# Performance work log

Hardware: AMD Instinct MI355X
Metric: run time of the kernel (lower is better)

The kernel has to match this reference:

```python
import jax, jax.numpy as jnp
import numpy as np

D, DH, NH = 256, 32, 8  # d_model, d_head, n_heads


def conv2d(x, w, stride=1, padding='VALID', groups=1):
    return jax.lax.conv_general_dilated(
        x, w, (stride, stride), padding,
        feature_group_count=groups,
        dimension_numbers=('NCHW', 'OIHW', 'NCHW'))


def bn2d(x, p):
    # p: [4, C] rows = gamma, beta, running_mean, running_var (inference-mode BN)
    g, b, m, v = p[0], p[1], p[2], p[3]
    inv = g / jnp.sqrt(v + 1e-5)
    return (x - m[:, None, None]) * inv[:, None, None] + b[:, None, None]


def gelu(x):
    return jax.nn.gelu(x, approximate=False)  # torch nn.GELU default (erf)


def to_heads(x):
    # [b, heads*d, h, w] -> [b, h*w, heads, d]
    b, c, h, w = x.shape
    return x.reshape(b, NH, DH, h * w).transpose(0, 3, 1, 2)


def from_heads(x, h, w):
    # [b, h*w, heads, d] -> [b, heads*d, h, w]
    b = x.shape[0]
    return x.transpose(0, 2, 3, 1).reshape(b, NH * DH, h, w)


def linear_attention(q, k, v, eps=1e-6):
    # LoFTR linear attention: phi(x) = elu(x) + 1
    Q = jax.nn.elu(q) + 1.0
    K = jax.nn.elu(k) + 1.0
    L = v.shape[1]
    vn = v / L
    KV = jnp.einsum('nshd,nshv->nhdv', K, vn)
    Z = 1.0 / (jnp.einsum('nlhd,nhd->nlh', Q, K.sum(axis=1)) + eps)
    return jnp.einsum('nlhd,nhdv,nlh->nlhv', Q, KV, Z) * L


def upsample_bilinear_ac(x, s):
    # bilinear, align_corners=True, integer scale factor s (separable H then W)
    def interp(a, axis):
        n_in = a.shape[axis]
        n_out = n_in * s
        pos = jnp.arange(n_out) * ((n_in - 1) / (n_out - 1))
        i0 = jnp.floor(pos).astype(jnp.int32)
        i1 = jnp.minimum(i0 + 1, n_in - 1)
        t = (pos - i0.astype(pos.dtype)).astype(a.dtype)
        sh = [1] * a.ndim
        sh[axis] = n_out
        t = t.reshape(sh)
        return jnp.take(a, i0, axis=axis) * (1 - t) + jnp.take(a, i1, axis=axis) * t
    return interp(interp(x, 2), 3)


def _bn_params(key, c):
    k1, k2, k3, k4 = jax.random.split(key, 4)
    return jnp.stack([
        1.0 + 0.05 * jax.random.normal(k1, (c,)),
        0.05 * jax.random.normal(k2, (c,)),
        0.05 * jax.random.normal(k3, (c,)),
        0.5 + jax.random.uniform(k4, (c,))]).astype(jnp.float32)


def setup_inputs() -> dict:
    key = jax.random.key(0)
    ks = jax.random.split(key, 24)
    B, H, W = 4, 128, 128
    Dm = 4 * D  # MB hidden dim (mlp_ratio=4)

    def w(k, shape, fan_in):
        return (jax.random.normal(k, shape) / np.sqrt(fan_in)).astype(jnp.float32)

    return {
        'x0': jax.random.normal(ks[0], (B, D, H, W), dtype=jnp.float32),
        'scale_weight': jnp.ones((3,), jnp.float32),
        'bn_pre': _bn_params(ks[1], D),
        'wq1': w(ks[2], (D, D, 1, 1), D),
        'wk1': w(ks[3], (D, D, 1, 1), D),
        'wv1': w(ks[4], (D, D, 1, 1), D),
        'wq2': w(ks[5], (D, D, 2, 2), D * 4),
        'wk2': w(ks[6], (D, D, 2, 2), D * 4),
        'wv2': w(ks[7], (D, D, 2, 2), D * 4),
        'wq3': w(ks[8], (D, D, 4, 4), D * 16),
        'wk3': w(ks[9], (D, D, 4, 4), D * 16),
        'wv3': w(ks[10], (D, D, 4, 4), D * 16),
        'merge_w': w(ks[11], (D, D, 1, 1), D),
        'merge_b': 0.01 * jax.random.normal(ks[12], (D,), dtype=jnp.float32),
        'mb_w1': w(ks[13], (Dm, D, 1, 1), D),
        'bn_mb1': _bn_params(ks[14], Dm),
        'mb_wdw': w(ks[15], (Dm, 1, 3, 3), 9),
        'bn_mb2': _bn_params(ks[16], Dm),
        'mb_w2': w(ks[17], (D, Dm, 1, 1), Dm),
        'bn_mb3': _bn_params(ks[18], D),
    }


def reference(x0, scale_weight, bn_pre, wq1, wk1, wv1, wq2, wk2, wv2,
              wq3, wk3, wv3, merge_w, merge_b, mb_w1, bn_mb1, mb_wdw,
              bn_mb2, mb_w2, bn_mb3):
    b, d, h, w = x0.shape
    xn = gelu(bn2d(x0, bn_pre))  # x1 is None -> x1 = x0, shared pre_normact
    # multi-scale conv QKV projections (strides 1, 2, 4)
    q1 = to_heads(conv2d(xn, wq1)); k1 = to_heads(conv2d(xn, wk1)); v1 = to_heads(conv2d(xn, wv1))
    q2 = to_heads(conv2d(xn, wq2, 2)); k2 = to_heads(conv2d(xn, wk2, 2)); v2 = to_heads(conv2d(xn, wv2, 2))
    q3 = to_heads(conv2d(xn, wq3, 4)); k3 = to_heads(conv2d(xn, wk3, 4)); v3 = to_heads(conv2d(xn, wv3, 4))
    o1 = from_heads(linear_attention(q1, k1, v1), h, w)
    o2 = from_heads(linear_attention(q2, k2, v2), h // 2, w // 2)
    o3 = from_heads(linear_attention(q3, k3, v3), h // 4, w // 4)
    o2 = upsample_bilinear_ac(o2, 2)
    o3 = upsample_bilinear_ac(o3, 4)
    sw = jax.nn.softmax(scale_weight)
    message = sw[0] * o1 + sw[1] * o2 + sw[2] * o3
    x = x0 + conv2d(message, merge_w) + merge_b[:, None, None]  # DropPath(0) = id
    # MB mlp: 1x1 expand -> BN -> GELU -> 3x3 depthwise -> BN -> GELU -> 1x1 -> BN
    hm = gelu(bn2d(conv2d(x, mb_w1), bn_mb1))
    hm = gelu(bn2d(conv2d(hm, mb_wdw, 1, ((1, 1), (1, 1)), groups=mb_wdw.shape[0]), bn_mb2))
    mlp_out = bn2d(conv2d(hm, mb_w2), bn_mb3)
    return x + mlp_out
```

## Files before the change

### kernel.cpp

```cpp
#include <hip/hip_runtime.h>
#include <hip/hip_bf16.h>

typedef __attribute__((ext_vector_type(4))) float f32x4;
typedef __attribute__((ext_vector_type(8))) short short8;
typedef unsigned int u32;
typedef unsigned short u16;

__device__ __forceinline__ float bf2f(u16 x) { return __uint_as_float(((u32)x) << 16); }
__device__ __forceinline__ u16 f2bf(float f) {
  u32 u = __float_as_uint(f);
  return (u16)((u + 0x7fffu + ((u >> 16) & 1u)) >> 16);
}
__device__ __forceinline__ float gelu_f(float x) { return 0.5f * x * (1.f + erff(x * 0.7071067811865475f)); }
__device__ __forceinline__ float phi_f(float x) { return x > 0.f ? x + 1.f : __expf(x); }
__device__ __forceinline__ void load8f(const __hip_bfloat16* p, float* f) {
  ushort4 a = *(const ushort4*)p, b = *(const ushort4*)(p + 4);
  f[0] = bf2f(a.x); f[1] = bf2f(a.y); f[2] = bf2f(a.z); f[3] = bf2f(a.w);
  f[4] = bf2f(b.x); f[5] = bf2f(b.y); f[6] = bf2f(b.z); f[7] = bf2f(b.w);
}
__device__ __forceinline__ void gload16(const void* g, void* l) {
  __builtin_amdgcn_global_load_lds((const __attribute__((address_space(1))) u32*)g,
                                   (__attribute__((address_space(3))) u32*)l, 16, 0, 0);
}

static constexpr size_t MiB = 1048576ull;
static constexpr size_t OFF_BNP_S = 0, OFF_BNP_T = 1024;
static constexpr size_t OFF_BN1_S = 2048, OFF_BN1_T = 6144;
static constexpr size_t OFF_BN2_S = 10240, OFF_BN2_T = 14336;
static constexpr size_t OFF_BN3_S = 18432, OFF_BN3_T = 19456;
static constexpr size_t OFF_WDW   = 20480;
static constexpr size_t OFF_KV    = 57344;
static constexpr size_t OFF_KSUM  = 450560;
static constexpr size_t OFF_W     = 524288;
static constexpr size_t WF1 = 0;
static constexpr size_t WF2 = 196608;
static constexpr size_t WF3 = 983040;
static constexpr size_t WE_MRG = 4128768;
static constexpr size_t WE_MB1 = 4194304;
static constexpr size_t WE_MB2 = 4456448;
static constexpr size_t OFF_XN    = 20 * MiB;
static constexpr size_t OFF_O1    = 52 * MiB;
static constexpr size_t OFF_O2    = 84 * MiB;
static constexpr size_t OFF_O3    = 92 * MiB;
static constexpr size_t OFF_QKV2  = 96 * MiB;
static constexpr size_t OFF_QKV3  = 120 * MiB;
static constexpr size_t OFF_PART  = 126 * MiB;
static constexpr size_t OFF_QKV1C = 126 * MiB;
static constexpr size_t OFF_MSG   = 128 * MiB;
static constexpr size_t OFF_XB    = 20 * MiB;
static constexpr size_t OFF_HM1   = 52 * MiB;
static constexpr size_t OFF_HM2   = 116 * MiB;
static constexpr size_t WS_NEED   = 180 * MiB;

__global__ __launch_bounds__(256) void fillf(float* p, int n, float v) {
  for (int i = blockIdx.x * 256 + threadIdx.x; i < n; i += gridDim.x * 256) p[i] = v;
}

__global__ __launch_bounds__(256) void bnprep(const float* __restrict__ bn,
                                              float* __restrict__ s, float* __restrict__ t, int C) {
  int c = blockIdx.x * 256 + threadIdx.x;
  if (c >= C) return;
  float g = bn[c], b = bn[C + c], m = bn[2 * C + c], v = bn[3 * C + c];
  float sc = g * rsqrtf(v + 1e-5f);
  s[c] = sc; t[c] = b - m * sc;
}

__global__ __launch_bounds__(256) void wdwprep(const float* __restrict__ w, float* __restrict__ out) {
  int g = blockIdx.x * 256 + threadIdx.x;
  if (g >= 9216) return;
  int c = g & 1023, p = g >> 10;
  out[p * 1024 + c] = w[c * 9 + p];
}

__global__ __launch_bounds__(256)
void wprep_all(const float* q1, const float* k1, const float* v1,
               const float* q2, const float* k2, const float* v2,
               const float* q3, const float* k3, const float* v3,
               const float* mrg, const float* m1, const float* m2,
               __hip_bfloat16* __restrict__ pool) {
  int g = blockIdx.x * 256 + threadIdx.x;
  if (g >= 4718592) return;
  const float* src; int C, S; int loc; size_t base;
  if (g < 196608)      { int seg = g / 65536;   src = seg == 0 ? q1 : seg == 1 ? k1 : v1; C = 256; S = 1; base = 0;       loc = g - seg * 65536; }
  else if (g < 983040) { int r = g - 196608; int seg = r / 262144; src = seg == 0 ? q2 : seg == 1 ? k2 : v2; C = 256; S = 2; base = 196608;  loc = r - seg * 262144; }
  else if (g < 4128768){ int r = g - 983040; int seg = r / 1048576; src = seg == 0 ? q3 : seg == 1 ? k3 : v3; C = 256; S = 4; base = 983040; loc = r - seg * 1048576; }
  else if (g < 4194304){ src = mrg; C = 256; S = 1; base = 4128768; loc = g - 4128768; }
  else if (g < 4456448){ src = m1; C = 256; S = 1; base = 4194304; loc = g - 4194304; }
  else                 { src = m2; C = 1024; S = 1; base = 4456448; loc = g - 4456448; }
  (void)base;
  int K = C * S * S;
  int o = loc / K, kk = loc - o * K;
  int c = kk % C, p = kk / C;
  pool[g] = __float2bfloat16(src[((size_t)o * C + c) * S * S + p]);
}

__global__ __launch_bounds__(256) void pre_normact(const float* __restrict__ x0, const float* __restrict__ s,
                                                   const float* __restrict__ t, __hip_bfloat16* __restrict__ xn) {
  __shared__ u16 lds[64 * 256];
  const int tid = threadIdx.x;
  const int p0 = blockIdx.x * 64;
  const int b = p0 >> 14, pin = p0 & 16383;
  const float sc = s[tid], sh = t[tid];
  const float* src = x0 + (((size_t)(b * 256 + tid)) << 14) + pin;
  #pragma unroll 4
  for (int j = 0; j < 64; j += 4) {
    float4 v = *(const float4*)(src + j);
    lds[(j + 0) * 256 + tid] = f2bf(gelu_f(v.x * sc + sh));
    lds[(j + 1) * 256 + tid] = f2bf(gelu_f(v.y * sc + sh));
    lds[(j + 2) * 256 + tid] = f2bf(gelu_f(v.z * sc + sh));
    lds[(j + 3) * 256 + tid] = f2bf(gelu_f(v.w * sc + sh));
  }
  __syncthreads();
  const uint4* lsrc = (const uint4*)lds;
  uint4* dst = (uint4*)((u16*)xn + (size_t)p0 * 256);
  #pragma unroll
  for (int i = 0; i < 8; ++i) dst[i * 256 + tid] = lsrc[i * 256 + tid];
}

template <int S, int EPI>
__global__ __launch_bounds__(256)
void gemm_bt(const __hip_bfloat16* __restrict__ A, const __hip_bfloat16* __restrict__ Bw,
             __hip_bfloat16* __restrict__ Cout, int N, int K, int ldb,
             const float* __restrict__ p0, const float* __restrict__ p1,
             const float* __restrict__ xsrc, float* __restrict__ xout, int ksplit) {
  __shared__ __hip_bfloat16 As[2][128 * 64];
  __shared__ __hip_bfloat16 Bs[2][128 * 64];
  const int tid = threadIdx.x;
  const int wave = tid >> 6, lane = tid & 63;
  const int ntn = N >> 7;
  int blk = blockIdx.x;
  { int nwg = gridDim.x; if ((nwg & 7) == 0) { int cpx = nwg >> 3; blk = (blk & 7) * cpx + (blk >> 3); } }
  int kbeg = 0, kend = K;
  float* xo = xout;
  if constexpr (EPI == 7) {
    int tiles = gridDim.x / ksplit;
    int split = blk / tiles; blk -= split * tiles;
    int knum = K / ksplit;
    kbeg = split * knum; kend = kbeg + knum;
    int M = (tiles / ntn) << 7;
    xo = xout + (size_t)split * M * N;
  }
  const int bm = blk / ntn, bnn = blk % ntn;
  const int wr = wave >> 1, wc = wave & 1;
  const int r_lo = lane & 15, r_hi = lane >> 4;
  f32x4 acc[4][4] = {};

  const __hip_bfloat16* aptr[4];
  #pragma unroll
  for (int i = 0; i < 4; ++i) {
    int ci = i * 256 + tid;
    int row = ci >> 3, c8 = ci & 7;
    int m = bm * 128 + row;
    size_t pixbase;
    if constexpr (S == 1) pixbase = (size_t)m * K;
    else if constexpr (S == 2) { int b = m >> 12, y = (m >> 6) & 63, x = m & 63; pixbase = ((size_t)(b * 16384 + y * 256 + x * 2)) * 256; }
    else { int b = m >> 10, y = (m >> 5) & 31, x = m & 31; pixbase = ((size_t)(b * 16384 + y * 512 + x * 4)) * 256; }
    aptr[i] = A + pixbase + c8 * 8;
  }
  const __hip_bfloat16* bptr[4];
  #pragma unroll
  for (int i = 0; i < 4; ++i) {
    int ci = i * 256 + tid;
    int row = ci >> 3, c8 = ci & 7;
    bptr[i] = Bw + (size_t)(bnn * 128 + row) * ldb + c8 * 8;
  }
  const int lofs = wave * 64 * 8;

  auto aoff_of = [&](int k0) -> size_t {
    if constexpr (S == 1) return (size_t)k0;
    else { int pq = k0 >> 8; int dy = pq / S, dx = pq % S; return (size_t)(((dy << 7) + dx) << 8) + (k0 & 255); }
  };

  {
    size_t ao = aoff_of(kbeg);
    #pragma unroll
    for (int i = 0; i < 4; ++i)
      gload16(aptr[i] + ao, (void*)(As[0] + i * 2048 + lofs));
    #pragma unroll
    for (int i = 0; i < 4; ++i)
      gload16(bptr[i] + kbeg, (void*)(Bs[0] + i * 2048 + lofs));
  }
  __syncthreads();

  int cur = 0;
  for (int k0 = kbeg; k0 < kend; k0 += 64) {
    if (k0 + 64 < kend) {
      size_t ao = aoff_of(k0 + 64);
      #pragma unroll
      for (int i = 0; i < 4; ++i)
        gload16(aptr[i] + ao, (void*)(As[cur ^ 1] + i * 2048 + lofs));
      #pragma unroll
      for (int i = 0; i < 4; ++i)
        gload16(bptr[i] + k0 + 64, (void*)(Bs[cur ^ 1] + i * 2048 + lofs));
    }
    const __hip_bfloat16* Ab = As[cur];
    const __hip_bfloat16* Bb = Bs[cur];
    #pragma unroll
    for (int kk = 0; kk < 2; ++kk) {
      short8 af[4], bfr[4];
      #pragma unroll
      for (int mi = 0; mi < 4; ++mi)
        af[mi] = *(const short8*)(Ab + (wr * 64 + mi * 16 + r_lo) * 64 + kk * 32 + r_hi * 8);
      #pragma unroll
      for (int ni = 0; ni < 4; ++ni)
        bfr[ni] = *(const short8*)(Bb + (wc * 64 + ni * 16 + r_lo) * 64 + kk * 32 + r_hi * 8);
      #pragma unroll
      for (int mi = 0; mi < 4; ++mi)
        #pragma unroll
        for (int ni = 0; ni < 4; ++ni)
          acc[mi][ni] = __builtin_amdgcn_mfma_f32_16x16x32_bf16(af[mi], bfr[ni], acc[mi][ni], 0, 0, 0);
    }
    __syncthreads();
    cur ^= 1;
  }

  const int m_base = bm * 128 + wr * 64;
  const int n_base = bnn * 128 + wc * 64;
  #pragma unroll
  for (int mi = 0; mi < 4; ++mi) {
    const int row0 = m_base + mi * 16 + r_hi * 4;
    #pragma unroll
    for (int ni = 0; ni < 4; ++ni) {
      const int col = n_base + ni * 16 + r_lo;
      f32x4 v = acc[mi][ni];
      if constexpr (EPI == 0) {
        #pragma unroll
        for (int j = 0; j < 4; ++j)
          *((u16*)Cout + (size_t)(row0 + j) * N + col) = f2bf(v[j]);
      } else if constexpr (EPI == 1) {
        const float sc = p0[col], sh = p1[col];
        #pragma unroll
        for (int j = 0; j < 4; ++j)
          *((u16*)Cout + (size_t)(row0 + j) * N + col) = f2bf(gelu_f(v[j] * sc + sh));
      } else if constexpr (EPI == 2) {
        const int b = row0 >> 14, pix = row0 & 16383;
        const size_t nchw = (((size_t)(b * 256 + col)) << 14) + pix;
        const float bias = p0[col];
        float4 xv = *(const float4*)(xsrc + nchw);
        float r0 = v[0] + bias + xv.x, r1 = v[1] + bias + xv.y;
        float r2 = v[2] + bias + xv.z, r3 = v[3] + bias + xv.w;
        *(float4*)(xo + nchw) = make_float4(r0, r1, r2, r3);
        *((u16*)Cout + (size_t)(row0 + 0) * 256 + col) = f2bf(r0);
        *((u16*)Cout + (size_t)(row0 + 1) * 256 + col) = f2bf(r1);
        *((u16*)Cout + (size_t)(row0 + 2) * 256 + col) = f2bf(r2);
        *((u16*)Cout + (size_t)(row0 + 3) * 256 + col) = f2bf(r3);
      } else if constexpr (EPI == 7) {
        #pragma unroll
        for (int j = 0; j < 4; ++j)
          xo[(size_t)(row0 + j) * N + col] = v[j];
      } else {
        const int b = row0 >> 14, pix = row0 & 16383;
        const size_t nchw = (((size_t)(b * 256 + col)) << 14) + pix;
        const float sc = p0[col], sh = p1[col];
        float4 pv = *(const float4*)(xo + nchw);
        *(float4*)(xo + nchw) = make_float4(v[0] * sc + sh + pv.x, v[1] * sc + sh + pv.y,
                                            v[2] * sc + sh + pv.z, v[3] * sc + sh + pv.w);
      }
    }
  }
}

__global__ __launch_bounds__(256) void reduce_part(const float* __restrict__ P,
                                                   __hip_bfloat16* __restrict__ out, int MN) {
  int i = (blockIdx.x * 256 + threadIdx.x) * 4;
  if (i >= MN) return;
  float4 a = *(const float4*)(P + i);
  float4 b = *(const float4*)(P + MN + i);
  ushort4 o;
  o.x = f2bf(a.x + b.x); o.y = f2bf(a.y + b.y); o.z = f2bf(a.z + b.z); o.w = f2bf(a.w + b.w);
  *(ushort4*)((u16*)out + i) = o;
}

__global__ __launch_bounds__(256)
void kv_reduce(const __hip_bfloat16* __restrict__ Km, const __hip_bfloat16* __restrict__ Vm,
               float* __restrict__ KV, float* __restrict__ Ksum, int L, int nchunks, int ld) {
  __shared__ float Ks[16][32];
  __shared__ float Vs[16][32];
  const int tid = threadIdx.x;
  const int blk = blockIdx.x;
  const int chunk = blk % nchunks;
  const int bh = blk / nchunks;
  const int h = bh & 7, b = bh >> 3;
  const int d = tid >> 3, v0 = (tid & 7) << 2;
  const int lr = tid >> 4, lq = tid & 15;
  const int cq = (lq & 7) << 2;
  const bool isK = lq < 8;
  const __hip_bfloat16* src = isK ? Km : Vm;
  const int CL = L / nchunks;
  const size_t base = (size_t)(b * L + chunk * CL) * ld + h * 32 + cq;
  float a0 = 0, a1 = 0, a2 = 0, a3 = 0, ks = 0;
  for (int it = 0; it < CL; it += 16) {
    ushort4 u = *(const ushort4*)(src + base + (size_t)(it + lr) * ld);
    float f0 = bf2f(u.x), f1 = bf2f(u.y), f2 = bf2f(u.z), f3 = bf2f(u.w);
    if (isK) {
      Ks[lr][cq + 0] = phi_f(f0); Ks[lr][cq + 1] = phi_f(f1);
      Ks[lr][cq + 2] = phi_f(f2); Ks[lr][cq + 3] = phi_f(f3);
    } else {
      Vs[lr][cq + 0] = f0; Vs[lr][cq + 1] = f1; Vs[lr][cq + 2] = f2; Vs[lr][cq + 3] = f3;
    }
    __syncthreads();
    #pragma unroll
    for (int s = 0; s < 16; ++s) {
      float kk = Ks[s][d];
      ks += kk;
      float4 vv = *(const float4*)&Vs[s][v0];
      a0 += kk * vv.x; a1 += kk * vv.y; a2 += kk * vv.z; a3 += kk * vv.w;
    }
    __syncthreads();
  }
  float* kvp = KV + (size_t)bh * 1024 + d * 32 + v0;
  atomicAdd(kvp + 0, a0); atomicAdd(kvp + 1, a1);
  atomicAdd(kvp + 2, a2); atomicAdd(kvp + 3, a3);
  if ((tid & 7) == 0) atomicAdd(Ksum + bh * 32 + d, ks);
}

__global__ __launch_bounds__(256)
void attn_out(const __hip_bfloat16* __restrict__ Qm, const float* __restrict__ KV,
              const float* __restrict__ Ksum, __hip_bfloat16* __restrict__ O, int npg, int ld) {
  __shared__ float QL[32][32];
  __shared__ float KVL[32][32];
  __shared__ float KsL[32];
  const int tid = threadIdx.x;
  const int blk = blockIdx.x;
  const int pg = blk % npg, bh = blk / npg;
  const int h = bh & 7;
  const int L = npg << 5;
  const int m0 = (bh >> 3) * L + (pg << 5);
  *(float4*)&KVL[tid >> 3][(tid & 7) * 4] = *(const float4*)(KV + (size_t)bh * 1024 + tid * 4);
  if (tid < 32) KsL[tid] = Ksum[bh * 32 + tid];
  {
    const int p = tid >> 3, d4 = (tid & 7) * 4;
    ushort4 qu = *(const ushort4*)(Qm + (size_t)(m0 + p) * ld + h * 32 + d4);
    *(float4*)&QL[p][d4] = make_float4(phi_f(bf2f(qu.x)), phi_f(bf2f(qu.y)),
                                       phi_f(bf2f(qu.z)), phi_f(bf2f(qu.w)));
  }
  __syncthreads();
  const int p = tid >> 3, v0 = (tid & 7) * 4;
  float a0 = 0, a1 = 0, a2 = 0, a3 = 0, z = 0;
  #pragma unroll 8
  for (int d = 0; d < 32; ++d) {
    float q = QL[p][d];
    z += q * KsL[d];
    float4 kv = *(const float4*)&KVL[d][v0];
    a0 += q * kv.x; a1 += q * kv.y; a2 += q * kv.z; a3 += q * kv.w;
  }
  float zi = 1.f / (z + 1e-6f);
  ushort4 o;
  o.x = f2bf(a0 * zi); o.y = f2bf(a1 * zi); o.z = f2bf(a2 * zi); o.w = f2bf(a3 * zi);
  *(ushort4*)(O + (size_t)(m0 + p) * 256 + h * 32 + v0) = o;
}

__global__ __launch_bounds__(256)
void message_compose(const __hip_bfloat16* __restrict__ o1, const __hip_bfloat16* __restrict__ o2,
                     const __hip_bfloat16* __restrict__ o3, const float* __restrict__ sw,
                     __hip_bfloat16* __restrict__ msg) {
  const int g = blockIdx.x * 256 + threadIdx.x;
  const int c0 = (g & 31) << 3;
  const int pix = g >> 5;
  const int x = pix & 127, y = (pix >> 7) & 127, b = pix >> 14;
  float w0 = sw[0], w1 = sw[1], w2 = sw[2];
  float mx = fmaxf(w0, fmaxf(w1, w2));
  float e0 = __expf(w0 - mx), e1 = __expf(w1 - mx), e2 = __expf(w2 - mx);
  float inv = 1.f / (e0 + e1 + e2);
  float s0 = e0 * inv, s1 = e1 * inv, s2 = e2 * inv;

  float acc[8], f[8];
  load8f(o1 + (size_t)pix * 256 + c0, f);
  #pragma unroll
  for (int j = 0; j < 8; ++j) acc[j] = s0 * f[j];
  {
    float py = y * (63.f / 127.f); int y0 = (int)py; float ty = py - y0; int y1 = min(y0 + 1, 63);
    float px = x * (63.f / 127.f); int x0 = (int)px; float tx = px - x0; int x1 = min(x0 + 1, 63);
    float wtl = (1 - ty) * (1 - tx), wtr = (1 - ty) * tx, wbl = ty * (1 - tx), wbr = ty * tx;
    const __hip_bfloat16* base = o2 + (size_t)b * 4096 * 256 + c0;
    float f00[8], f01[8], f10[8], f11[8];
    load8f(base + ((size_t)y0 * 64 + x0) * 256, f00);
    load8f(base + ((size_t)y0 * 64 + x1) * 256, f01);
    load8f(base + ((size_t)y1 * 64 + x0) * 256, f10);
    load8f(base + ((size_t)y1 * 64 + x1) * 256, f11);
    #pragma unroll
    for (int j = 0; j < 8; ++j)
      acc[j] += s1 * (wtl * f00[j] + wtr * f01[j] + wbl * f10[j] + wbr * f11[j]);
  }
  {
    float py = y * (31.f / 127.f); int y0 = (int)py; float ty = py - y0; int y1 = min(y0 + 1, 31);
    float px = x * (31.f / 127.f); int x0 = (int)px; float tx = px - x0; int x1 = min(x0 + 1, 31);
    float wtl = (1 - ty) * (1 - tx), wtr = (1 - ty) * tx, wbl = ty * (1 - tx), wbr = ty * tx;
    const __hip_bfloat16* base = o3 + (size_t)b * 1024 * 256 + c0;
    float f00[8], f01[8], f10[8], f11[8];
    load8f(base + ((size_t)y0 * 32 + x0) * 256, f00);
    load8f(base + ((size_t)y0 * 32 + x1) * 256, f01);
    load8f(base + ((size_t)y1 * 32 + x0) * 256, f10);
    load8f(base + ((size_t)y1 * 32 + x1) * 256, f11);
    #pragma unroll
    for (int j = 0; j < 8; ++j)
      acc[j] += s2 * (wtl * f00[j] + wtr * f01[j] + wbl * f10[j] + wbr * f11[j]);
  }
  ushort4 oa, ob;
  oa.x = f2bf(acc[0]); oa.y = f2bf(acc[1]); oa.z = f2bf(acc[2]); oa.w = f2bf(acc[3]);
  ob.x = f2bf(acc[4]); ob.y = f2bf(acc[5]); ob.z = f2bf(acc[6]); ob.w = f2bf(acc[7]);
  *(ushort4*)(msg + (size_t)pix * 256 + c0) = oa;
  *(ushort4*)(msg + (size_t)pix * 256 + c0 + 4) = ob;
}

__global__ __launch_bounds__(256)
void dwconv(const __hip_bfloat16* __restrict__ hm1, const float* __restrict__ wdw,
            const float* __restrict__ s, const float* __restrict__ t, __hip_bfloat16* __restrict__ hm2) {
  const int g = blockIdx.x * 256 + threadIdx.x;
  const int c0 = (g & 127) << 3;
  const int pix = g >> 7;
  const int x = pix & 127, y = (pix >> 7) & 127, b = pix >> 14;
  float acc[8] = {0, 0, 0, 0, 0, 0, 0, 0};
  #pragma unroll
  for (int ky = 0; ky < 3; ++ky) {
    int yy = y + ky - 1;
    if ((unsigned)yy >= 128u) continue;
    #pragma unroll
    for (int kx = 0; kx < 3; ++kx) {
      int xx = x + kx - 1;
      if ((unsigned)xx >= 128u) continue;
      const __hip_bfloat16* p = hm1 + ((((size_t)b * 128 + yy) * 128 + xx) << 10) + c0;
      ushort4 ua = *(const ushort4*)p, ub = *(const ushort4*)(p + 4);
      float4 wa = *(const float4*)&wdw[(ky * 3 + kx) * 1024 + c0];
      float4 wb = *(const float4*)&wdw[(ky * 3 + kx) * 1024 + c0 + 4];
      acc[0] += bf2f(ua.x) * wa.x; acc[1] += bf2f(ua.y) * wa.y;
      acc[2] += bf2f(ua.z) * wa.z; acc[3] += bf2f(ua.w) * wa.w;
      acc[4] += bf2f(ub.x) * wb.x; acc[5] += bf2f(ub.y) * wb.y;
      acc[6] += bf2f(ub.z) * wb.z; acc[7] += bf2f(ub.w) * wb.w;
    }
  }
  float4 sa = *(const float4*)&s[c0], sb = *(const float4*)&s[c0 + 4];
  float4 ta = *(const float4*)&t[c0], tb = *(const float4*)&t[c0 + 4];
  ushort4 oa, ob;
  oa.x = f2bf(gelu_f(acc[0] * sa.x + ta.x)); oa.y = f2bf(gelu_f(acc[1] * sa.y + ta.y));
  oa.z = f2bf(gelu_f(acc[2] * sa.z + ta.z)); oa.w = f2bf(gelu_f(acc[3] * sa.w + ta.w));
  ob.x = f2bf(gelu_f(acc[4] * sb.x + tb.x)); ob.y = f2bf(gelu_f(acc[5] * sb.y + tb.y));
  ob.z = f2bf(gelu_f(acc[6] * sb.z + tb.z)); ob.w = f2bf(gelu_f(acc[7] * sb.w + tb.w));
  *(ushort4*)(hm2 + ((size_t)pix << 10) + c0) = oa;
  *(ushort4*)(hm2 + ((size_t)pix << 10) + c0 + 4) = ob;
}

extern "C" void kernel_launch(void* const* d_in, const int* in_sizes, int n_in,
                              void* d_out, int out_size, void* d_ws, size_t ws_size,
                              hipStream_t stream) {
  const float* x0      = (const float*)d_in[0];
  const float* scale_w = (const float*)d_in[1];
  const float* bn_pre  = (const float*)d_in[2];
  const float* wq1 = (const float*)d_in[3];
  const float* wk1 = (const float*)d_in[4];
  const float* wv1 = (const float*)d_in[5];
  const float* wq2 = (const float*)d_in[6];
  const float* wk2 = (const float*)d_in[7];
  const float* wv2 = (const float*)d_in[8];
  const float* wq3 = (const float*)d_in[9];
  const float* wk3 = (const float*)d_in[10];
  const float* wv3 = (const float*)d_in[11];
  const float* merge_w = (const float*)d_in[12];
  const float* merge_b = (const float*)d_in[13];
  const float* mb_w1   = (const float*)d_in[14];
  const float* bn_mb1  = (const float*)d_in[15];
  const float* mb_wdw  = (const float*)d_in[16];
  const float* bn_mb2  = (const float*)d_in[17];
  const float* mb_w2   = (const float*)d_in[18];
  const float* bn_mb3  = (const float*)d_in[19];
  (void)in_sizes; (void)n_in;

  if (ws_size < WS_NEED) {
    fillf<<<4096, 256, 0, stream>>>((float*)d_out, out_size, (float)(ws_size >> 20));
    return;
  }

  char* ws = (char*)d_ws;
  auto F  = [&](size_t off) { return (float*)(ws + off); };
  auto BF = [&](size_t off) { return (__hip_bfloat16*)(ws + off); };
  __hip_bfloat16* Wp = BF(OFF_W);
  float* KV = F(OFF_KV);
  float* KS = F(OFF_KSUM);
  float* Xout = (float*)d_out;

  bnprep<<<1, 256, 0, stream>>>(bn_pre, F(OFF_BNP_S), F(OFF_BNP_T), 256);
  bnprep<<<4, 256, 0, stream>>>(bn_mb1, F(OFF_BN1_S), F(OFF_BN1_T), 1024);
  bnprep<<<4, 256, 0, stream>>>(bn_mb2, F(OFF_BN2_S), F(OFF_BN2_T), 1024);
  bnprep<<<1, 256, 0, stream>>>(bn_mb3, F(OFF_BN3_S), F(OFF_BN3_T), 256);
  wdwprep<<<36, 256, 0, stream>>>(mb_wdw, F(OFF_WDW));
  wprep_all<<<18432, 256, 0, stream>>>(wq1, wk1, wv1, wq2, wk2, wv2, wq3, wk3, wv3,
                                       merge_w, mb_w1, mb_w2, Wp);
  hipMemsetAsync(ws + OFF_KV, 0, 405504, stream);

  pre_normact<<<1024, 256, 0, stream>>>(x0, F(OFF_BNP_S), F(OFF_BNP_T), BF(OFF_XN));

  gemm_bt<2, 0><<<768, 256, 0, stream>>>(BF(OFF_XN), Wp + WF2, BF(OFF_QKV2), 768, 1024, 1024,
                                         nullptr, nullptr, nullptr, nullptr, 1);
  gemm_bt<4, 7><<<384, 256, 0, stream>>>(BF(OFF_XN), Wp + WF3, nullptr, 768, 4096, 4096,
                                         nullptr, nullptr, nullptr, F(OFF_PART), 2);
  reduce_part<<<3072, 256, 0, stream>>>(F(OFF_PART), BF(OFF_QKV3), 4096 * 768);

  kv_reduce<<<256, 256, 0, stream>>>(BF(OFF_QKV2) + 256, BF(OFF_QKV2) + 512, KV + 32768, KS + 1024, 4096, 8, 768);
  kv_reduce<<<256, 256, 0, stream>>>(BF(OFF_QKV3) + 256, BF(OFF_QKV3) + 512, KV + 65536, KS + 2048, 1024, 8, 768);
  attn_out<<<4096, 256, 0, stream>>>(BF(OFF_QKV2), KV + 32768, KS + 1024, BF(OFF_O2), 128, 768);
  attn_out<<<1024, 256, 0, stream>>>(BF(OFF_QKV3), KV + 65536, KS + 2048, BF(OFF_O3), 32, 768);

  for (int c = 0; c < 4; ++c) {
    const __hip_bfloat16* Ac = BF(OFF_XN) + (size_t)c * 16384 * 256;
    gemm_bt<1, 0><<<768, 256, 0, stream>>>(Ac, Wp + WF1, BF(OFF_QKV1C), 768, 256, 256,
                                           nullptr, nullptr, nullptr, nullptr, 1);
    kv_reduce<<<512, 256, 0, stream>>>(BF(OFF_QKV1C) + 256, BF(OFF_QKV1C) + 512,
                                       KV + c * 8192, KS + c * 256, 16384, 64, 768);
    attn_out<<<4096, 256, 0, stream>>>(BF(OFF_QKV1C), KV + c * 8192, KS + c * 256,
                                       BF(OFF_O1) + (size_t)c * 16384 * 256, 512, 768);
  }

  message_compose<<<8192, 256, 0, stream>>>(BF(OFF_O1), BF(OFF_O2), BF(OFF_O3), scale_w, BF(OFF_MSG));
  gemm_bt<1, 2><<<1024, 256, 0, stream>>>(BF(OFF_MSG), Wp + WE_MRG, BF(OFF_XB), 256, 256, 256,
                                          merge_b, nullptr, x0, Xout, 1);

  for (int half = 0; half < 2; ++half) {
    const __hip_bfloat16* XBh = BF(OFF_XB) + (size_t)half * 32768 * 256;
    float* Xoh = Xout + (size_t)half * 2 * 256 * 16384;
    gemm_bt<1, 1><<<2048, 256, 0, stream>>>(XBh, Wp + WE_MB1, BF(OFF_HM1), 1024, 256, 256,
                                            F(OFF_BN1_S), F(OFF_BN1_T), nullptr, nullptr, 1);
    dwconv<<<16384, 256, 0, stream>>>(BF(OFF_HM1), F(OFF_WDW), F(OFF_BN2_S), F(OFF_BN2_T), BF(OFF_HM2));
    gemm_bt<1, 8><<<512, 256, 0, stream>>>(BF(OFF_HM2), Wp + WE_MB2, nullptr, 256, 1024, 1024,
                                           F(OFF_BN3_S), F(OFF_BN3_T), nullptr, Xoh, 1);
  }
}
```

Baseline: 1.047 ms.

## Restructure attn_out per-pixel all-heads, row-streaming dwconv, fold BN scale, larger QKV1 chunks

attn_out now has each thread compute all 32 output channels for one pixel and head, with the KV matrices for all 8 heads staged in padded LDS. This removes the per-head-block Q staging and uses fewer, larger blocks. dwconv streams down 16-row column segments per thread, keeping the weights in registers and reusing each loaded row for three output rows, which cuts redundant global loads. The BN2 scale is folded into the depthwise weights at prep time, and the QKV1 path is processed in 2 chunks of 2 images instead of 4, with MSG aliased onto the freed workspace. Register pressure rises (q[32], acc[32], w[72]) and dwconv parallelism drops to 256K threads.

```diff
diff --git a/kernel.cpp b/kernel.cpp
--- a/kernel.cpp
+++ b/kernel.cpp
@@ -17,6 +17,12 @@
   ushort4 a = *(const ushort4*)p, b = *(const ushort4*)(p + 4);
   f[0] = bf2f(a.x); f[1] = bf2f(a.y); f[2] = bf2f(a.z); f[3] = bf2f(a.w);
   f[4] = bf2f(b.x); f[5] = bf2f(b.y); f[6] = bf2f(b.z); f[7] = bf2f(b.w);
+}
+__device__ __forceinline__ void cvt8(uint4 u, float* f) {
+  f[0] = bf2f((u16)(u.x & 0xffff)); f[1] = bf2f((u16)(u.x >> 16));
+  f[2] = bf2f((u16)(u.y & 0xffff)); f[3] = bf2f((u16)(u.y >> 16));
+  f[4] = bf2f((u16)(u.z & 0xffff)); f[5] = bf2f((u16)(u.z >> 16));
+  f[6] = bf2f((u16)(u.w & 0xffff)); f[7] = bf2f((u16)(u.w >> 16));
 }
 __device__ __forceinline__ void gload16(const void* g, void* l) {
   __builtin_amdgcn_global_load_lds((const __attribute__((address_space(1))) u32*)g,
@@ -45,8 +51,8 @@
 static constexpr size_t OFF_QKV2  = 96 * MiB;
 static constexpr size_t OFF_QKV3  = 120 * MiB;
 static constexpr size_t OFF_PART  = 126 * MiB;
-static constexpr size_t OFF_QKV1C = 126 * MiB;
-static constexpr size_t OFF_MSG   = 128 * MiB;
+static constexpr size_t OFF_QKV1P = 126 * MiB;
+static constexpr size_t OFF_MSG   = 126 * MiB;
 static constexpr size_t OFF_XB    = 20 * MiB;
 static constexpr size_t OFF_HM1   = 52 * MiB;
 static constexpr size_t OFF_HM2   = 116 * MiB;
@@ -65,11 +71,12 @@
   s[c] = sc; t[c] = b - m * sc;
 }
 
-__global__ __launch_bounds__(256) void wdwprep(const float* __restrict__ w, float* __restrict__ out) {
+__global__ __launch_bounds__(256) void wdwprep(const float* __restrict__ w, const float* __restrict__ s,
+                                               float* __restrict__ out) {
   int g = blockIdx.x * 256 + threadIdx.x;
   if (g >= 9216) return;
   int c = g & 1023, p = g >> 10;
-  out[p * 1024 + c] = w[c * 9 + p];
+  out[p * 1024 + c] = w[c * 9 + p] * s[c];
 }
 
 __global__ __launch_bounds__(256)
@@ -80,14 +87,13 @@
                __hip_bfloat16* __restrict__ pool) {
   int g = blockIdx.x * 256 + threadIdx.x;
   if (g >= 4718592) return;
-  const float* src; int C, S; int loc; size_t base;
-  if (g < 196608)      { int seg = g / 65536;   src = seg == 0 ? q1 : seg == 1 ? k1 : v1; C = 256; S = 1; base = 0;       loc = g - seg * 65536; }
-  else if (g < 983040) { int r = g - 196608; int seg = r / 262144; src = seg == 0 ? q2 : seg == 1 ? k2 : v2; C = 256; S = 2; base = 196608;  loc = r - seg * 262144; }
-  else if (g < 4128768){ int r = g - 983040; int seg = r / 1048576; src = seg == 0 ? q3 : seg == 1 ? k3 : v3; C = 256; S = 4; base = 983040; loc = r - seg * 1048576; }
-  else if (g < 4194304){ src = mrg; C = 256; S = 1; base = 4128768; loc = g - 4128768; }
-  else if (g < 4456448){ src = m1; C = 256; S = 1; base = 4194304; loc = g - 4194304; }
-  else                 { src = m2; C = 1024; S = 1; base = 4456448; loc = g - 4456448; }
-  (void)base;
+  const float* src; int C, S; int loc;
+  if (g < 196608)      { int seg = g / 65536;   src = seg == 0 ? q1 : seg == 1 ? k1 : v1; C = 256; S = 1; loc = g - seg * 65536; }
+  else if (g < 983040) { int r = g - 196608; int seg = r / 262144; src = seg == 0 ? q2 : seg == 1 ? k2 : v2; C = 256; S = 2; loc = r - seg * 262144; }
+  else if (g < 4128768){ int r = g - 983040; int seg = r / 1048576; src = seg == 0 ? q3 : seg == 1 ? k3 : v3; C = 256; S = 4; loc = r - seg * 1048576; }
+  else if (g < 4194304){ src = mrg; C = 256; S = 1; loc = g - 4128768; }
+  else if (g < 4456448){ src = m1; C = 256; S = 1; loc = g - 4194304; }
+  else                 { src = m2; C = 1024; S = 1; loc = g - 4456448; }
   int K = C * S * S;
   int o = loc / K, kk = loc - o * K;
   int c = kk % C, p = kk / C;
@@ -316,38 +322,59 @@
 
 __global__ __launch_bounds__(256)
 void attn_out(const __hip_bfloat16* __restrict__ Qm, const float* __restrict__ KV,
-              const float* __restrict__ Ksum, __hip_bfloat16* __restrict__ O, int npg, int ld) {
-  __shared__ float QL[32][32];
-  __shared__ float KVL[32][32];
-  __shared__ float KsL[32];
+              const float* __restrict__ Ksum, __hip_bfloat16* __restrict__ O, int lshift, int ld) {
+  __shared__ float KVL[8 * 1156];
+  __shared__ float KsL[8 * 33];
   const int tid = threadIdx.x;
-  const int blk = blockIdx.x;
-  const int pg = blk % npg, bh = blk / npg;
-  const int h = bh & 7;
-  const int L = npg << 5;
-  const int m0 = (bh >> 3) * L + (pg << 5);
-  *(float4*)&KVL[tid >> 3][(tid & 7) * 4] = *(const float4*)(KV + (size_t)bh * 1024 + tid * 4);
-  if (tid < 32) KsL[tid] = Ksum[bh * 32 + tid];
-  {
-    const int p = tid >> 3, d4 = (tid & 7) * 4;
-    ushort4 qu = *(const ushort4*)(Qm + (size_t)(m0 + p) * ld + h * 32 + d4);
-    *(float4*)&QL[p][d4] = make_float4(phi_f(bf2f(qu.x)), phi_f(bf2f(qu.y)),
-                                       phi_f(bf2f(qu.z)), phi_f(bf2f(qu.w)));
+  const int m0 = blockIdx.x << 5;
+  const int bh0 = (m0 >> lshift) << 3;
+  #pragma unroll
+  for (int i = 0; i < 8; ++i) {
+    int id = i * 256 + tid;
+    int h = id >> 8, rem = id & 255;
+    int d = rem >> 3, vi = rem & 7;
+    float4 v = *(const float4*)(KV + (((size_t)(bh0 + h)) << 10) + rem * 4);
+    *(float4*)&KVL[h * 1156 + d * 36 + vi * 4] = v;
+  }
+  { int h = tid >> 5, d = tid & 31; KsL[h * 33 + d] = Ksum[(bh0 + h) * 32 + d]; }
+  const int p = tid >> 3, h = tid & 7;
+  const u16* qp = (const u16*)Qm + (size_t)(m0 + p) * ld + h * 32;
+  float q[32];
+  #pragma unroll
+  for (int i = 0; i < 4; ++i) {
+    uint4 u = *(const uint4*)(qp + i * 8);
+    q[i * 8 + 0] = phi_f(bf2f((u16)(u.x & 0xffff))); q[i * 8 + 1] = phi_f(bf2f((u16)(u.x >> 16)));
+    q[i * 8 + 2] = phi_f(bf2f((u16)(u.y & 0xffff))); q[i * 8 + 3] = phi_f(bf2f((u16)(u.y >> 16)));
+    q[i * 8 + 4] = phi_f(bf2f((u16)(u.z & 0xffff))); q[i * 8 + 5] = phi_f(bf2f((u16)(u.z >> 16)));
+    q[i * 8 + 6] = phi_f(bf2f((u16)(u.w & 0xffff))); q[i * 8 + 7] = phi_f(bf2f((u16)(u.w >> 16)));
   }
   __syncthreads();
-  const int p = tid >> 3, v0 = (tid & 7) * 4;
-  float a0 = 0, a1 = 0, a2 = 0, a3 = 0, z = 0;
-  #pragma unroll 8
+  const float* kvh = &KVL[h * 1156];
+  const float* ksh = &KsL[h * 33];
+  float acc[32] = {};
+  float z = 0.f;
+  #pragma unroll
   for (int d = 0; d < 32; ++d) {
-    float q = QL[p][d];
-    z += q * KsL[d];
-    float4 kv = *(const float4*)&KVL[d][v0];
-    a0 += q * kv.x; a1 += q * kv.y; a2 += q * kv.z; a3 += q * kv.w;
+    float qd = q[d];
+    z += qd * ksh[d];
+    #pragma unroll
+    for (int vi = 0; vi < 8; ++vi) {
+      float4 kv = *(const float4*)&kvh[d * 36 + vi * 4];
+      acc[vi * 4 + 0] += qd * kv.x; acc[vi * 4 + 1] += qd * kv.y;
+      acc[vi * 4 + 2] += qd * kv.z; acc[vi * 4 + 3] += qd * kv.w;
+    }
   }
   float zi = 1.f / (z + 1e-6f);
-  ushort4 o;
-  o.x = f2bf(a0 * zi); o.y = f2bf(a1 * zi); o.z = f2bf(a2 * zi); o.w = f2bf(a3 * zi);
-  *(ushort4*)(O + (size_t)(m0 + p) * 256 + h * 32 + v0) = o;
+  u16* op = (u16*)O + (size_t)(m0 + p) * 256 + h * 32;
+  #pragma unroll
+  for (int i = 0; i < 4; ++i) {
+    uint4 o;
+    o.x = (u32)f2bf(acc[i * 8 + 0] * zi) | ((u32)f2bf(acc[i * 8 + 1] * zi) << 16);
+    o.y = (u32)f2bf(acc[i * 8 + 2] * zi) | ((u32)f2bf(acc[i * 8 + 3] * zi) << 16);
+    o.z = (u32)f2bf(acc[i * 8 + 4] * zi) | ((u32)f2bf(acc[i * 8 + 5] * zi) << 16);
+    o.w = (u32)f2bf(acc[i * 8 + 6] * zi) | ((u32)f2bf(acc[i * 8 + 7] * zi) << 16);
+    *(uint4*)(op + i * 8) = o;
+  }
 }
 
 __global__ __launch_bounds__(256)
@@ -405,39 +432,58 @@
 
 __global__ __launch_bounds__(256)
 void dwconv(const __hip_bfloat16* __restrict__ hm1, const float* __restrict__ wdw,
-            const float* __restrict__ s, const float* __restrict__ t, __hip_bfloat16* __restrict__ hm2) {
+            const float* __restrict__ t, __hip_bfloat16* __restrict__ hm2) {
   const int g = blockIdx.x * 256 + threadIdx.x;
   const int c0 = (g & 127) << 3;
-  const int pix = g >> 7;
-  const int x = pix & 127, y = (pix >> 7) & 127, b = pix >> 14;
-  float acc[8] = {0, 0, 0, 0, 0, 0, 0, 0};
-  #pragma unroll
-  for (int ky = 0; ky < 3; ++ky) {
-    int yy = y + ky - 1;
-    if ((unsigned)yy >= 128u) continue;
-    #pragma unroll
-    for (int kx = 0; kx < 3; ++kx) {
-      int xx = x + kx - 1;
-      if ((unsigned)xx >= 128u) continue;
-      const __hip_bfloat16* p = hm1 + ((((size_t)b * 128 + yy) * 128 + xx) << 10) + c0;
-      ushort4 ua = *(const ushort4*)p, ub = *(const ushort4*)(p + 4);
-      float4 wa = *(const float4*)&wdw[(ky * 3 + kx) * 1024 + c0];
-      float4 wb = *(const float4*)&wdw[(ky * 3 + kx) * 1024 + c0 + 4];
-      acc[0] += bf2f(ua.x) * wa.x; acc[1] += bf2f(ua.y) * wa.y;
-      acc[2] += bf2f(ua.z) * wa.z; acc[3] += bf2f(ua.w) * wa.w;
-      acc[4] += bf2f(ub.x) * wb.x; acc[5] += bf2f(ub.y) * wb.y;
-      acc[6] += bf2f(ub.z) * wb.z; acc[7] += bf2f(ub.w) * wb.w;
-    }
-  }
-  float4 sa = *(const float4*)&s[c0], sb = *(const float4*)&s[c0 + 4];
-  float4 ta = *(const float4*)&t[c0], tb = *(const float4*)&t[c0 + 4];
-  ushort4 oa, ob;
-  oa.x = f2bf(gelu_f(acc[0] * sa.x + ta.x)); oa.y = f2bf(gelu_f(acc[1] * sa.y + ta.y));
-  oa.z = f2bf(gelu_f(acc[2] * sa.z + ta.z)); oa.w = f2bf(gelu_f(acc[3] * sa.w + ta.w));
-  ob.x = f2bf(gelu_f(acc[4] * sb.x + tb.x)); ob.y = f2bf(gelu_f(acc[5] * sb.y + tb.y));
-  ob.z = f2bf(gelu_f(acc[6] * sb.z + tb.z)); ob.w = f2bf(gelu_f(acc[7] * sb.w + tb.w));
-  *(ushort4*)(hm2 + ((size_t)pix << 10) + c0) = oa;
-  *(ushort4*)(hm2 + ((size_t)pix << 10) + c0 + 4) = ob;
+  const int x = (g >> 7) & 127;
+  const int seg = (g >> 14) & 7;
+  const int img = g >> 17;
+  const int y0 = seg << 4;
+  const bool hasL = x > 0, hasR = x < 127;
+
+  float w[9][8];
+  #pragma unroll
+  for (int t9 = 0; t9 < 9; ++t9) {
+    *(float4*)&w[t9][0] = *(const float4*)&wdw[t9 * 1024 + c0];
+    *(float4*)&w[t9][4] = *(const float4*)&wdw[t9 * 1024 + c0 + 4];
+  }
+  float tb[8];
+  *(float4*)&tb[0] = *(const float4*)&t[c0];
+  *(float4*)&tb[4] = *(const float4*)&t[c0 + 4];
+
+  const __hip_bfloat16* rb = hm1 + (((size_t)(img * 16384 + x)) << 10) + c0;
+  __hip_bfloat16* ob = hm2 + (((size_t)(img * 16384 + x)) << 10) + c0;
+  const uint4 zz = make_uint4(0, 0, 0, 0);
+
+  float A[8] = {}, B[8] = {};
+  for (int r = y0 - 1; r <= y0 + 16; ++r) {
+    float l[8], m[8], rv[8];
+    uint4 ul = zz, um = zz, ur = zz;
+    if ((unsigned)r < 128u) {
+      const __hip_bfloat16* pr = rb + ((size_t)r << 17);
+      um = *(const uint4*)pr;
+      if (hasL) ul = *(const uint4*)(pr - 1024);
+      if (hasR) ur = *(const uint4*)(pr + 1024);
+    }
+    cvt8(ul, l); cvt8(um, m); cvt8(ur, rv);
+    if (r > y0) {
+      u16 o[8];
+      #pragma unroll
+      for (int j = 0; j < 8; ++j) {
+        float fin = A[j] + w[6][j] * l[j] + w[7][j] * m[j] + w[8][j] * rv[j];
+        o[j] = f2bf(gelu_f(fin + tb[j]));
+      }
+      *(uint4*)(ob + ((size_t)(r - 1) << 17)) = *(uint4*)o;
+    }
+    if (r < y0 + 16) {
+      #pragma unroll
+      for (int j = 0; j < 8; ++j) {
+        float na = B[j] + w[3][j] * l[j] + w[4][j] * m[j] + w[5][j] * rv[j];
+        B[j] = w[0][j] * l[j] + w[1][j] * m[j] + w[2][j] * rv[j];
+        A[j] = na;
+      }
+    }
+  }
 }
 
 extern "C" void kernel_launch(void* const* d_in, const int* in_sizes, int n_in,
@@ -482,7 +528,7 @@
   bnprep<<<4, 256, 0, stream>>>(bn_mb1, F(OFF_BN1_S), F(OFF_BN1_T), 1024);
   bnprep<<<4, 256, 0, stream>>>(bn_mb2, F(OFF_BN2_S), F(OFF_BN2_T), 1024);
   bnprep<<<1, 256, 0, stream>>>(bn_mb3, F(OFF_BN3_S), F(OFF_BN3_T), 256);
-  wdwprep<<<36, 256, 0, stream>>>(mb_wdw, F(OFF_WDW));
+  wdwprep<<<36, 256, 0, stream>>>(mb_wdw, F(OFF_BN2_S), F(OFF_WDW));
   wprep_all<<<18432, 256, 0, stream>>>(wq1, wk1, wv1, wq2, wk2, wv2, wq3, wk3, wv3,
                                        merge_w, mb_w1, mb_w2, Wp);
   hipMemsetAsync(ws + OFF_KV, 0, 405504, stream);
@@ -497,17 +543,17 @@
 
   kv_reduce<<<256, 256, 0, stream>>>(BF(OFF_QKV2) + 256, BF(OFF_QKV2) + 512, KV + 32768, KS + 1024, 4096, 8, 768);
   kv_reduce<<<256, 256, 0, stream>>>(BF(OFF_QKV3) + 256, BF(OFF_QKV3) + 512, KV + 65536, KS + 2048, 1024, 8, 768);
-  attn_out<<<4096, 256, 0, stream>>>(BF(OFF_QKV2), KV + 32768, KS + 1024, BF(OFF_O2), 128, 768);
-  attn_out<<<1024, 256, 0, stream>>>(BF(OFF_QKV3), KV + 65536, KS + 2048, BF(OFF_O3), 32, 768);
-
-  for (int c = 0; c < 4; ++c) {
-    const __hip_bfloat16* Ac = BF(OFF_XN) + (size_t)c * 16384 * 256;
-    gemm_bt<1, 0><<<768, 256, 0, stream>>>(Ac, Wp + WF1, BF(OFF_QKV1C), 768, 256, 256,
-                                           nullptr, nullptr, nullptr, nullptr, 1);
-    kv_reduce<<<512, 256, 0, stream>>>(BF(OFF_QKV1C) + 256, BF(OFF_QKV1C) + 512,
-                                       KV + c * 8192, KS + c * 256, 16384, 64, 768);
-    attn_out<<<4096, 256, 0, stream>>>(BF(OFF_QKV1C), KV + c * 8192, KS + c * 256,
-                                       BF(OFF_O1) + (size_t)c * 16384 * 256, 512, 768);
+  attn_out<<<512, 256, 0, stream>>>(BF(OFF_QKV2), KV + 32768, KS + 1024, BF(OFF_O2), 12, 768);
+  attn_out<<<128, 256, 0, stream>>>(BF(OFF_QKV3), KV + 65536, KS + 2048, BF(OFF_O3), 10, 768);
+
+  for (int c = 0; c < 2; ++c) {
+    const __hip_bfloat16* Ac = BF(OFF_XN) + (size_t)c * 32768 * 256;
+    gemm_bt<1, 0><<<1536, 256, 0, stream>>>(Ac, Wp + WF1, BF(OFF_QKV1P), 768, 256, 256,
+                                            nullptr, nullptr, nullptr, nullptr, 1);
+    kv_reduce<<<512, 256, 0, stream>>>(BF(OFF_QKV1P) + 256, BF(OFF_QKV1P) + 512,
+                                       KV + c * 16384, KS + c * 512, 16384, 32, 768);
+    attn_out<<<1024, 256, 0, stream>>>(BF(OFF_QKV1P), KV + c * 16384, KS + c * 512,
+                                       BF(OFF_O1) + (size_t)c * 32768 * 256, 14, 768);
   }
 
   message_compose<<<8192, 256, 0, stream>>>(BF(OFF_O1), BF(OFF_O2), BF(OFF_O3), scale_w, BF(OFF_MSG));
@@ -519,7 +565,7 @@
     float* Xoh = Xout + (size_t)half * 2 * 256 * 16384;
     gemm_bt<1, 1><<<2048, 256, 0, stream>>>(XBh, Wp + WE_MB1, BF(OFF_HM1), 1024, 256, 256,
                                             F(OFF_BN1_S), F(OFF_BN1_T), nullptr, nullptr, 1);
-    dwconv<<<16384, 256, 0, stream>>>(BF(OFF_HM1), F(OFF_WDW), F(OFF_BN2_S), F(OFF_BN2_T), BF(OFF_HM2));
+    dwconv<<<1024, 256, 0, stream>>>(BF(OFF_HM1), F(OFF_WDW), F(OFF_BN2_T), BF(OFF_HM2));
     gemm_bt<1, 8><<<512, 256, 0, stream>>>(BF(OFF_HM2), Wp + WE_MB2, nullptr, 256, 1024, 1024,
                                            F(OFF_BN3_S), F(OFF_BN3_T), nullptr, Xoh, 1);
   }
```

New measurement: 951.1 us. 1.1x faster.
